# Performance work log

Hardware: AMD Instinct MI355X
Metric: run time of the kernel (lower is better)

Reference implementation:

```python
import jax, jax.numpy as jnp
import numpy as np

B, C, H, W = 4, 256, 32, 32
N_HEADS, N_GROUPS = 8, 4
HEAD_C = C // N_HEADS            # 32
GROUP_C = C // N_GROUPS          # 64
GROUP_HEADS = N_HEADS // N_GROUPS  # 2
OFFSET_RANGE_FACTOR = 4.0
SCALE = HEAD_C ** -0.5
EPS = 1e-5


def grid_sample(img, grid):
    """Bilinear grid_sample, align_corners=True, zeros padding.
    img: (N, Ch, Hi, Wi); grid: (N, Hg, Wg, 2) with (x, y) in [-1, 1]."""
    N, Ch, Hi, Wi = img.shape
    x = (grid[..., 0] + 1.0) * 0.5 * (Wi - 1)
    y = (grid[..., 1] + 1.0) * 0.5 * (Hi - 1)
    x0 = jnp.floor(x); y0 = jnp.floor(y)
    x1 = x0 + 1.0; y1 = y0 + 1.0
    wx1 = x - x0; wx0 = 1.0 - wx1
    wy1 = y - y0; wy0 = 1.0 - wy1
    img_flat = img.reshape(N, Ch, Hi * Wi)

    def corner(xi, yi, w):
        valid = (xi >= 0) & (xi <= Wi - 1) & (yi >= 0) & (yi <= Hi - 1)
        xc = jnp.clip(xi, 0, Wi - 1).astype(jnp.int32)
        yc = jnp.clip(yi, 0, Hi - 1).astype(jnp.int32)
        idx = yc * Wi + xc  # (N, Hg, Wg)
        vals = jax.vmap(lambda im, ix: im[:, ix])(img_flat, idx)  # (N, Ch, Hg, Wg)
        return vals * (w * valid)[:, None, :, :]

    return (corner(x0, y0, wx0 * wy0) + corner(x1, y0, wx1 * wy0)
            + corner(x0, y1, wx0 * wy1) + corner(x1, y1, wx1 * wy1))


def setup_inputs() -> dict:
    key = jax.random.key(0)
    ks = jax.random.split(key, 12)
    s = C ** -0.5
    return {
        "q_feat": jax.random.normal(ks[0], (B, C, H, W), jnp.float32),
        "kv_feat": jax.random.normal(ks[1], (B, C, H, W), jnp.float32),
        "Wq": jax.random.normal(ks[2], (C, C), jnp.float32) * s,
        "bq": jnp.zeros((C,), jnp.float32),
        "Wk": jax.random.normal(ks[3], (C, C), jnp.float32) * s,
        "bk": jnp.zeros((C,), jnp.float32),
        "Wv": jax.random.normal(ks[4], (C, C), jnp.float32) * s,
        "bv": jnp.zeros((C,), jnp.float32),
        "Wo": jax.random.normal(ks[5], (C, C), jnp.float32) * s,
        "bo": jnp.zeros((C,), jnp.float32),
        "off_dw_w": jax.random.normal(ks[6], (GROUP_C, 1, 3, 3), jnp.float32) / 3.0,
        "off_dw_b": jnp.zeros((GROUP_C,), jnp.float32),
        "off_ln_w": jnp.ones((GROUP_C,), jnp.float32),
        "off_ln_b": jnp.zeros((GROUP_C,), jnp.float32),
        "off_pw_w": jax.random.normal(ks[7], (2, GROUP_C), jnp.float32) * GROUP_C ** -0.5,
        "rpe_table": jax.random.normal(ks[8], (N_HEADS, 2 * H - 1, 2 * W - 1), jnp.float32) * 0.01,
    }


def reference(q_feat, kv_feat, Wq, bq, Wk, bk, Wv, bv, Wo, bo,
              off_dw_w, off_dw_b, off_ln_w, off_ln_b, off_pw_w, rpe_table):
    Bg = B * N_GROUPS
    n = H * W
    # q projection (1x1 conv)
    q = jnp.einsum('oi,bihw->bohw', Wq, q_feat) + bq[:, None, None]
    # offset network on grouped q
    q_off = q.reshape(Bg, GROUP_C, H, W)
    x = jax.lax.conv_general_dilated(q_off, off_dw_w, (1, 1), ((1, 1), (1, 1)),
                                     feature_group_count=GROUP_C,
                                     dimension_numbers=('NCHW', 'OIHW', 'NCHW'))
    x = x + off_dw_b[:, None, None]
    mu = x.mean(1, keepdims=True)
    var = x.var(1, keepdims=True)
    x = (x - mu) / jnp.sqrt(var + EPS) * off_ln_w[:, None, None] + off_ln_b[:, None, None]
    x = jax.nn.gelu(x, approximate=False)
    offset = jnp.einsum('oc,bchw->bohw', off_pw_w, x)  # (Bg, 2, H, W), (y, x)
    off_range = jnp.array([1.0 / (H - 1), 1.0 / (W - 1)], jnp.float32).reshape(1, 2, 1, 1)
    offset = jnp.tanh(offset) * off_range * OFFSET_RANGE_FACTOR
    offset = offset.transpose(0, 2, 3, 1)  # (Bg, H, W, 2)
    # reference points in [-1, 1]
    ref_y = (jnp.linspace(0.5, H - 0.5, H) / (H - 1.0)) * 2.0 - 1.0
    ref_x = (jnp.linspace(0.5, W - 0.5, W) / (W - 1.0)) * 2.0 - 1.0
    ref = jnp.stack(jnp.meshgrid(ref_y, ref_x, indexing='ij'), -1)  # (H, W, 2)
    pos = offset + ref[None]  # (Bg, H, W, 2), (y, x), no clamp (offset_range_factor >= 0)
    # deformable sampling of kv features
    kv_g = kv_feat.reshape(Bg, GROUP_C, H, W)
    x_sampled = grid_sample(kv_g, pos[..., ::-1]).reshape(B, C, n)
    k = jnp.einsum('oi,bin->bon', Wk, x_sampled) + bk[:, None]
    v = jnp.einsum('oi,bin->bon', Wv, x_sampled) + bv[:, None]
    qf = q.reshape(B, N_HEADS, HEAD_C, n)
    kf = k.reshape(B, N_HEADS, HEAD_C, n)
    vf = v.reshape(B, N_HEADS, HEAD_C, n)
    attn = jnp.einsum('bhcm,bhcn->bhmn', qf, kf) * SCALE
    # relative-position bias via bilinear sampling of rpe table
    gy = (jnp.arange(H, dtype=jnp.float32) / (H - 1.0)) * 2.0 - 1.0
    gx = (jnp.arange(W, dtype=jnp.float32) / (W - 1.0)) * 2.0 - 1.0
    q_grid = jnp.stack(jnp.meshgrid(gy, gx, indexing='ij'), -1).reshape(n, 2)
    pos_flat = pos.reshape(Bg, n, 2)
    disp = (q_grid[None, :, None, :] - pos_flat[:, None, :, :]) * 0.5  # (Bg, m, n, 2)
    rpe = jnp.broadcast_to(
        rpe_table.reshape(1, N_GROUPS, GROUP_HEADS, 2 * H - 1, 2 * W - 1),
        (B, N_GROUPS, GROUP_HEADS, 2 * H - 1, 2 * W - 1)
    ).reshape(Bg, GROUP_HEADS, 2 * H - 1, 2 * W - 1)
    bias = grid_sample(rpe, disp[..., ::-1])  # (Bg, GROUP_HEADS, m, n)
    attn = attn + bias.reshape(B, N_HEADS, n, n)
    attn = jax.nn.softmax(attn, axis=-1)
    out = jnp.einsum('bhmn,bhcn->bhcm', attn, vf).reshape(B, C, H, W)
    out = jnp.einsum('oi,bihw->bohw', Wo, out) + bo[:, None, None]
    return out
```

## Files before the change

### kernel.cpp

```cpp
#include <hip/hip_runtime.h>
#include <hip/hip_bf16.h>
#include <math.h>
#include <stdint.h>

#define BB 4
#define CC 256
#define HH 32
#define WW 32
#define NPIX 1024
#define NHEADS 8
#define NGROUPS 4
#define HEADC 32
#define GROUPC 64
#define BG 16
#define RPE_N 3969
#define SCALE_QK 0.17677669529663687f
#define LN_EPS 1e-5f

#define W_Q   0
#define W_POS 1048576
#define W_XS  1081344
#define W_KT  2129920
#define W_VV  2654208
#define W_AO  3178496
#define W_RPE 4227072
#define W_WSP 4264608

#define RPE_PACKED 4692

using frag  = __attribute__((ext_vector_type(8))) short;
using f32x4 = __attribute__((ext_vector_type(4))) float;

struct InPtrs { const void* p[16]; };

__device__ __forceinline__ float tof(float x){ return x; }
__device__ __forceinline__ float tof(__hip_bfloat16 x){ return __bfloat162float(x); }
__device__ __forceinline__ short bfs(float v) {
  __hip_bfloat16 h = __float2bfloat16(v);
  return *(short*)&h;
}
__device__ __forceinline__ bool is_f32(const void* lnw) {
  return *(const unsigned int*)lnw == 0x3F800000u;
}
__device__ __forceinline__ float ldm(const void* p, size_t i, bool f32m) {
  return f32m ? ((const float*)p)[i] : __bfloat162float(((const __hip_bfloat16*)p)[i]);
}
__device__ __forceinline__ float lof(uint32_t g){ return __uint_as_float(g << 16); }
__device__ __forceinline__ float hif(uint32_t g){ return __uint_as_float(g & 0xffff0000u); }

__global__ __launch_bounds__(512)
void prep_kernel(InPtrs ip, uint32_t* __restrict__ rpeg,
                 unsigned short* __restrict__ wsp) {
  bool f32m = is_f32(ip.p[12]);
  int blk = blockIdx.x;
  int tid = threadIdx.x;
  if (blk < 8) {
    int h = blk;
    const size_t rbase = (size_t)h * RPE_N;
    uint32_t* dst = rpeg + (size_t)h * RPE_PACKED;
    for (int i = tid; i < 68 * 69; i += 512) {
      int r = i / 69, c = i - r * 69;
      int y = r - 3, x = c - 3;
      bool yv = (y >= 0) & (y < 63);
      float va = (yv & (x >= 0) & (x < 63)) ? ldm(ip.p[15], rbase + y * 63 + x, f32m) : 0.0f;
      float vb2 = (yv & (x >= -1) & (x < 62)) ? ldm(ip.p[15], rbase + y * 63 + x + 1, f32m) : 0.0f;
      __hip_bfloat16 ha = __float2bfloat16(va), hb = __float2bfloat16(vb2);
      dst[i] = (uint32_t)*(unsigned short*)&ha | ((uint32_t)*(unsigned short*)&hb << 16);
    }
  } else {
    int wb = blk - 8;
    const void* srcs[4] = { ip.p[2], ip.p[4], ip.p[6], ip.p[8] };
    int idx0 = wb * 4096 + tid * 8;
    int m = idx0 >> 16, e0 = idx0 & 65535;
    const void* src = srcs[m];
    unsigned short* hi = wsp + (size_t)m * 131072;
    unsigned short* lo = hi + 65536;
    #pragma unroll
    for (int j = 0; j < 8; ++j) {
      float w = ldm(src, e0 + j, f32m);
      __hip_bfloat16 h = __float2bfloat16(w);
      hi[e0 + j] = *(unsigned short*)&h;
      lo[e0 + j] = (unsigned short)bfs(w - __bfloat162float(h));
    }
  }
}

template<int TM>
__device__ __forceinline__ void gemm_body(const void* xsrc, bool xf32,
    const unsigned short* __restrict__ wsp, int b, int o0, int mb,
    short* Bs, f32x4* acc) {
  const int tid = threadIdx.x;
  const int wave = tid >> 6, lane = tid & 63, quad = lane >> 4, l15 = lane & 15;
  const int og = wave & 3, mh = wave >> 2;
  const int MS = TM >> 5;
  const int NE = TM >> 4;

  size_t gbase[NE];
  int lbase[NE];
  #pragma unroll
  for (int it = 0; it < NE; ++it) {
    int i = tid + 512 * it;
    int mm = i & (TM - 1), kk = i / TM;
    gbase[it] = ((size_t)(b * CC + kk)) * NPIX + mb + mm;
    lbase[it] = mm * 72 + ((((kk >> 3) ^ (mm & 3))) << 4) + (kk & 7);
  }

  float v[NE];
  #pragma unroll
  for (int it = 0; it < NE; ++it)
    v[it] = xf32 ? ((const float*)xsrc)[gbase[it]]
                 : __bfloat162float(((const __hip_bfloat16*)xsrc)[gbase[it]]);

  for (int s = 0; s < 8; ++s) {
    short* buf = Bs + (s & 1) * (TM * 72);
    #pragma unroll
    for (int it = 0; it < NE; ++it) {
      __hip_bfloat16 h = __float2bfloat16(v[it]);
      buf[lbase[it]] = *(short*)&h;
      buf[lbase[it] + 8] = bfs(v[it] - __bfloat162float(h));
    }
    if (s < 7) {
      size_t koff = (size_t)(s + 1) * 32 * NPIX;
      #pragma unroll
      for (int it = 0; it < NE; ++it)
        v[it] = xf32 ? ((const float*)xsrc)[gbase[it] + koff]
                     : __bfloat162float(((const __hip_bfloat16*)xsrc)[gbase[it] + koff]);
    }
    const int k0 = s * 32;
    size_t wofs = (size_t)(o0 + og * 16 + l15) * CC + k0 + quad * 8;
    frag wh = *(const frag*)(wsp + wofs);
    frag wl = *(const frag*)(wsp + 65536 + wofs);
    __syncthreads();
    #pragma unroll
    for (int ms = 0; ms < MS; ++ms) {
      int ml = mh * (TM >> 1) + ms * 16 + l15;
      const short* bp = buf + ml * 72 + ((quad ^ (ml & 3)) << 4);
      frag bh = *(const frag*)bp;
      frag bl = *(const frag*)(bp + 8);
      acc[ms] = __builtin_amdgcn_mfma_f32_16x16x32_bf16(wh, bh, acc[ms], 0, 0, 0);
      acc[ms] = __builtin_amdgcn_mfma_f32_16x16x32_bf16(wh, bl, acc[ms], 0, 0, 0);
      acc[ms] = __builtin_amdgcn_mfma_f32_16x16x32_bf16(wl, bh, acc[ms], 0, 0, 0);
    }
  }
}

__global__ __launch_bounds__(512)
void qproj_kernel(InPtrs ip, const unsigned short* __restrict__ wsp,
                  float* __restrict__ q) {
  __shared__ __align__(16) short Bs[2 * 32 * 72];
  bool f32m = is_f32(ip.p[12]);
  int mb = blockIdx.x * 32, o0 = blockIdx.y * 64, b = blockIdx.z;
  int tid = threadIdx.x;
  int wave = tid >> 6, lane = tid & 63, quad = lane >> 4, l15 = lane & 15;
  f32x4 acc[1] = {{0.f,0.f,0.f,0.f}};
  gemm_body<32>(ip.p[0], f32m, wsp, b, o0, mb, Bs, acc);
  int og = wave & 3, mh = wave >> 2;
  int od = o0 + og * 16 + quad * 4;
  float bv[4];
  #pragma unroll
  for (int r = 0; r < 4; ++r) bv[r] = ldm(ip.p[3], od + r, f32m);
  int m = mb + mh * 16 + l15;
  #pragma unroll
  for (int r = 0; r < 4; ++r)
    q[(size_t)(b * CC + od + r) * NPIX + m] = acc[0][r] + bv[r];
}

__global__ __launch_bounds__(512)
void kvproj_kernel(InPtrs ip, const unsigned short* __restrict__ wspal,
                   const float* __restrict__ xs,
                   __hip_bfloat16* __restrict__ kT, __hip_bfloat16* __restrict__ vbf) {
  __shared__ __align__(16) char arena[2 * 64 * 72 * 2];
  bool f32m = is_f32(ip.p[12]);
  int mt = blockIdx.x, ot = blockIdx.y, b = blockIdx.z;
  int mb = mt * 64;
  bool isV = (ot >= 4);
  int o0 = (ot & 3) * 64;
  const unsigned short* wsp = wspal + (size_t)(isV ? 2 : 1) * 131072;
  const void* braw = isV ? ip.p[7] : ip.p[5];
  int tid = threadIdx.x;
  int wave = tid >> 6, lane = tid & 63, quad = lane >> 4, l15 = lane & 15;
  f32x4 acc[2] = {{0.f,0.f,0.f,0.f},{0.f,0.f,0.f,0.f}};
  gemm_body<64>(xs, true, wsp, b, o0, mb, (short*)arena, acc);
  int og = wave & 3, mh = wave >> 2;
  int od = o0 + og * 16 + quad * 4;
  float bv[4];
  #pragma unroll
  for (int r = 0; r < 4; ++r) bv[r] = ldm(braw, od + r, f32m);
  if (isV) {
    #pragma unroll
    for (int ms = 0; ms < 2; ++ms) {
      int m = mb + mh * 32 + ms * 16 + l15;
      #pragma unroll
      for (int r = 0; r < 4; ++r)
        vbf[(size_t)(b * CC + od + r) * NPIX + m] = __float2bfloat16(acc[ms][r] + bv[r]);
    }
  } else {
    __syncthreads();
    float* Ds = (float*)arena;
    #pragma unroll
    for (int ms = 0; ms < 2; ++ms) {
      int ml = mh * 32 + ms * 16 + l15;
      #pragma unroll
      for (int r = 0; r < 4; ++r)
        Ds[(og * 16 + quad * 4 + r) * 65 + ml] = acc[ms][r] + bv[r];
    }
    __syncthreads();
    int ot4 = ot & 3;
    {
      int q2 = tid;
      int m = q2 >> 3, cc = q2 & 7;
      __hip_bfloat16 t8[8];
      #pragma unroll
      for (int j = 0; j < 8; ++j)
        t8[j] = __float2bfloat16(Ds[(cc * 8 + j) * 65 + m]);
      int h = ot4 * 2 + (cc >> 2);
      size_t addr = ((size_t)(b * NHEADS + h) * NPIX + mb + m) * HEADC + (cc & 3) * 8;
      *(uint4*)((short*)kT + addr) = *(const uint4*)t8;
    }
  }
}

__global__ __launch_bounds__(512)
void oproj_kernel(InPtrs ip, const unsigned short* __restrict__ wsp,
                  const float* __restrict__ ao, void* __restrict__ out) {
  __shared__ __align__(16) short Bs[2 * 32 * 72];
  bool f32m = is_f32(ip.p[12]);
  int mb = blockIdx.x * 32, o0 = blockIdx.y * 64, b = blockIdx.z;
  int tid = threadIdx.x;
  int wave = tid >> 6, lane = tid & 63, quad = lane >> 4, l15 = lane & 15;
  f32x4 acc[1] = {{0.f,0.f,0.f,0.f}};
  gemm_body<32>(ao, true, wsp, b, o0, mb, Bs, acc);
  int og = wave & 3, mh = wave >> 2;
  int od = o0 + og * 16 + quad * 4;
  float bv[4];
  #pragma unroll
  for (int r = 0; r < 4; ++r) bv[r] = ldm(ip.p[9], od + r, f32m);
  int m = mb + mh * 16 + l15;
  #pragma unroll
  for (int r = 0; r < 4; ++r) {
    float val = acc[0][r] + bv[r];
    size_t idx = (size_t)(b * CC + od + r) * NPIX + m;
    if (f32m) ((float*)out)[idx] = val;
    else      ((__hip_bfloat16*)out)[idx] = __float2bfloat16(val);
  }
}

template<typename T>
__device__ __forceinline__ float tap4(const T* __restrict__ img,
                                      int x0, int y0,
                                      float wx0, float wx1, float wy0, float wy1) {
  bool xv0 = (x0 >= 0) & (x0 < WW);
  bool xv1 = (x0 >= -1) & (x0 < WW - 1);
  bool yv0 = (y0 >= 0) & (y0 < HH);
  bool yv1 = (y0 >= -1) & (y0 < HH - 1);
  float acc = 0.0f;
  if (xv0 & yv0) acc += wx0 * wy0 * tof(img[y0 * WW + x0]);
  if (xv1 & yv0) acc += wx1 * wy0 * tof(img[y0 * WW + x0 + 1]);
  if (xv0 & yv1) acc += wx0 * wy1 * tof(img[(y0 + 1) * WW + x0]);
  if (xv1 & yv1) acc += wx1 * wy1 * tof(img[(y0 + 1) * WW + x0 + 1]);
  return acc;
}

__global__ __launch_bounds__(512)
void offsample_kernel(InPtrs ip, const float* __restrict__ q,
                      float* __restrict__ pos, float* __restrict__ xs) {
  __shared__ float qs[96][65];
  __shared__ float posl[64];
  bool f32m = is_f32(ip.p[12]);
  int blk = blockIdx.x;
  int hh = blk & 31, bg = blk >> 5;
  int b = bg >> 2, g = bg & 3;
  int tid = threadIdx.x;
  const float* qg = q + (size_t)(b * CC + g * GROUPC) * NPIX;
  #pragma unroll
  for (int k = 0; k < 12; ++k) {
    int idx = tid + 512 * k;
    int ww = idx & 31, c = (idx >> 5) & 63, r3 = idx >> 11;
    int yy = hh - 1 + r3;
    float v = (yy >= 0 && yy < HH) ? qg[(size_t)c * NPIX + yy * WW + ww] : 0.0f;
    qs[r3 * 32 + ww][c] = v;
  }
  __syncthreads();
  {
    int wave = tid >> 6, c = tid & 63;
    float wdw[9];
    #pragma unroll
    for (int j = 0; j < 9; ++j) wdw[j] = ldm(ip.p[10], c * 9 + j, f32m);
    float bdw = ldm(ip.p[11], c, f32m);
    float lnw = ldm(ip.p[12], c, f32m), lnb = ldm(ip.p[13], c, f32m);
    float pwy = ldm(ip.p[14], c, f32m), pwx = ldm(ip.p[14], GROUPC + c, f32m);

    for (int p4 = 0; p4 < 4; ++p4) {
      int ww = wave * 4 + p4;
      float x = bdw;
      #pragma unroll
      for (int dy = 0; dy < 3; ++dy)
        #pragma unroll
        for (int dx = 0; dx < 3; ++dx) {
          int xx = ww + dx - 1;
          if (xx >= 0 && xx < WW) x += wdw[dy * 3 + dx] * qs[dy * 32 + xx][c];
        }
      float s = x, s2 = x * x;
      #pragma unroll
      for (int off = 32; off > 0; off >>= 1) {
        s  += __shfl_xor(s,  off);
        s2 += __shfl_xor(s2, off);
      }
      float mu  = s * (1.0f / 64.0f);
      float var = s2 * (1.0f / 64.0f) - mu * mu;
      float xn = (x - mu) * (1.0f / sqrtf(var + LN_EPS)) * lnw + lnb;
      float ge = 0.5f * xn * (1.0f + erff(xn * 0.70710678118654752f));
      float oy = pwy * ge, ox = pwx * ge;
      #pragma unroll
      for (int off = 32; off > 0; off >>= 1) {
        oy += __shfl_xor(oy, off);
        ox += __shfl_xor(ox, off);
      }
      if (c == 0) {
        float fy = tanhf(oy) * (4.0f / 31.0f);
        float fx = tanhf(ox) * (4.0f / 31.0f);
        float ry = ((0.5f + (float)hh) / 31.0f) * 2.0f - 1.0f;
        float rx = ((0.5f + (float)ww) / 31.0f) * 2.0f - 1.0f;
        float py = fy + ry, px = fx + rx;
        int m = hh * 32 + ww;
        pos[((size_t)bg * NPIX + m) * 2 + 0] = py;
        pos[((size_t)bg * NPIX + m) * 2 + 1] = px;
        posl[ww * 2 + 0] = py;
        posl[ww * 2 + 1] = px;
      }
    }
  }
  __syncthreads();
  #pragma unroll
  for (int k = 0; k < 4; ++k) {
    int s = tid + 512 * k;
    int ww = s & 31, c = (s >> 5) & 63;
    float py = posl[ww * 2 + 0], px = posl[ww * 2 + 1];
    float xi = (px + 1.0f) * 15.5f, yi = (py + 1.0f) * 15.5f;
    float x0f = floorf(xi), y0f = floorf(yi);
    float wx1 = xi - x0f, wx0 = 1.0f - wx1;
    float wy1 = yi - y0f, wy0 = 1.0f - wy1;
    int x0 = (int)x0f, y0 = (int)y0f;
    size_t img_off = (size_t)(b * CC + g * GROUPC + c) * NPIX;
    float acc;
    if (f32m) acc = tap4((const float*)ip.p[1] + img_off, x0, y0, wx0, wx1, wy0, wy1);
    else      acc = tap4((const __hip_bfloat16*)ip.p[1] + img_off, x0, y0, wx0, wx1, wy0, wy1);
    xs[img_off + hh * 32 + ww] = acc;
  }
}

__global__ __launch_bounds__(512, 3)
void attn_mfma_kernel(InPtrs ip, const uint32_t* __restrict__ rpeg,
                      const float* __restrict__ q,
                      const __hip_bfloat16* __restrict__ kT,
                      const __hip_bfloat16* __restrict__ vbf,
                      const float* __restrict__ pos, float* __restrict__ ao) {
  __shared__ __align__(16) uint32_t Du[RPE_PACKED];
  __shared__ __align__(16) __hip_bfloat16 Pw[8][16][72];
  __shared__ __align__(16) __hip_bfloat16 qA[16][40];
  __shared__ float redmax[8 * 16];
  __shared__ float redsum[8 * 16];

  int bh = blockIdx.x;
  int b = bh >> 3, h = bh & 7;
  int m0 = blockIdx.y * 16;
  int tid = threadIdx.x;
  int bg = b * 4 + (h >> 1);

  size_t slice = (size_t)(b * CC + h * HEADC) * NPIX;
  const short* kTb = (const short*)kT + (size_t)bh * NPIX * HEADC;
  const short* vb = (const short*)vbf + slice;
  const float* qb = q + slice;
  const float* posb = pos + (size_t)bg * NPIX * 2;

  {
    const uint4* src = (const uint4*)(rpeg + (size_t)h * RPE_PACKED);
    uint4* dst = (uint4*)Du;
    for (int i = tid; i < 1173; i += 512) dst[i] = src[i];
  }
  {
    int r = tid & 15, c = tid >> 4;
    qA[r][c] = __float2bfloat16(qb[(size_t)c * NPIX + m0 + r] * SCALE_QK);
  }
  __syncthreads();

  int wave = tid >> 6, lane = tid & 63;
  int quad = lane >> 4, l15 = lane & 15;
  int nbase = wave * 128;

  frag aq = *(const frag*)&qA[l15][quad * 8];
  float ybase = 31.0f + 15.5f * ((float)(m0 >> 5) * (2.0f / 31.0f) - 1.0f);
  float xbase0 = 31.0f + 15.5f * ((float)(m0 & 31) * (2.0f / 31.0f) - 1.0f);

  float pm[4], ps[4];
  f32x4 acc0 = {0.f,0.f,0.f,0.f}, acc1 = {0.f,0.f,0.f,0.f};
  #pragma unroll
  for (int reg = 0; reg < 4; ++reg) { pm[reg] = -1e30f; ps[reg] = 0.0f; }

  #pragma unroll
  for (int half = 0; half < 2; ++half) {
    int hbase = nbase + half * 64;
    float sreg[4][4];
    #pragma unroll
    for (int t8 = 0; t8 < 4; ++t8) {
      int n = hbase + t8 * 16 + l15;
      frag bk = *(const frag*)(kTb + (size_t)n * HEADC + quad * 8);
      f32x4 d = __builtin_amdgcn_mfma_f32_16x16x32_bf16(aq, bk, (f32x4){0.f,0.f,0.f,0.f}, 0, 0, 0);
      float2 pp = *(const float2*)(posb + 2 * n);
      float yi = ybase - 15.5f * pp.x;
      float y0f = floorf(yi);
      float wy1 = yi - y0f, wy0 = 1.0f - wy1;
      float xi0 = xbase0 - 15.5f * pp.y;
      float x0f = floorf(xi0);
      float wx1 = xi0 - x0f, wx0 = 1.0f - wx1;
      int row = (int)y0f + 3;
      int col = (int)x0f + 3 + quad * 4;
      const uint32_t* Dp = Du + row * 69 + col;
      uint32_t g0 = Dp[0],  g1 = Dp[2],  g2 = Dp[4];
      uint32_t h0 = Dp[69], h1 = Dp[71], h2 = Dp[73];
      float u[5];
      u[0] = wy0 * lof(g0) + wy1 * lof(h0);
      u[1] = wy0 * hif(g0) + wy1 * hif(h0);
      u[2] = wy0 * lof(g1) + wy1 * lof(h1);
      u[3] = wy0 * hif(g1) + wy1 * hif(h1);
      u[4] = wy0 * lof(g2) + wy1 * lof(h2);
      #pragma unroll
      for (int reg = 0; reg < 4; ++reg)
        sreg[t8][reg] = d[reg] + wx0 * u[reg] + wx1 * u[reg + 1];
    }
    #pragma unroll
    for (int reg = 0; reg < 4; ++reg) {
      float m = fmaxf(fmaxf(sreg[0][reg], sreg[1][reg]),
                      fmaxf(sreg[2][reg], sreg[3][reg]));
      m = fmaxf(m, __shfl_xor(m, 1));
      m = fmaxf(m, __shfl_xor(m, 2));
      m = fmaxf(m, __shfl_xor(m, 4));
      m = fmaxf(m, __shfl_xor(m, 8));
      float newm = fmaxf(pm[reg], m);
      float sc = __expf(pm[reg] - newm);
      pm[reg] = newm;
      ps[reg] *= sc;
      acc0[reg] *= sc;
      acc1[reg] *= sc;
    }
    #pragma unroll
    for (int t8 = 0; t8 < 4; ++t8) {
      #pragma unroll
      for (int reg = 0; reg < 4; ++reg) {
        float p = __expf(sreg[t8][reg] - pm[reg]);
        Pw[wave][quad * 4 + reg][t8 * 16 + l15] = __float2bfloat16(p);
        ps[reg] += p;
      }
    }
    #pragma unroll
    for (int ks = 0; ks < 2; ++ks) {
      int koff = hbase + ks * 32 + quad * 8;
      frag ap = *(const frag*)&Pw[wave][l15][ks * 32 + quad * 8];
      frag bv0 = *(const frag*)(vb + (size_t)l15 * NPIX + koff);
      frag bv1 = *(const frag*)(vb + (size_t)(16 + l15) * NPIX + koff);
      acc0 = __builtin_amdgcn_mfma_f32_16x16x32_bf16(ap, bv0, acc0, 0, 0, 0);
      acc1 = __builtin_amdgcn_mfma_f32_16x16x32_bf16(ap, bv1, acc1, 0, 0, 0);
    }
  }

  #pragma unroll
  for (int reg = 0; reg < 4; ++reg) {
    ps[reg] += __shfl_xor(ps[reg], 1);
    ps[reg] += __shfl_xor(ps[reg], 2);
    ps[reg] += __shfl_xor(ps[reg], 4);
    ps[reg] += __shfl_xor(ps[reg], 8);
  }
  if (l15 == 0) {
    #pragma unroll
    for (int reg = 0; reg < 4; ++reg) {
      redmax[wave * 16 + quad * 4 + reg] = pm[reg];
      redsum[wave * 16 + quad * 4 + reg] = ps[reg];
    }
  }
  __syncthreads();

  float* part = (float*)&Pw[0][0][0];
  {
    int e0 = (0 * 16 + l15) * 16 + quad * 4;
    int e1 = (1 * 16 + l15) * 16 + quad * 4;
    #pragma unroll
    for (int reg = 0; reg < 4; ++reg) {
      part[wave * 512 + e0 + reg] = acc0[reg];
      part[wave * 512 + e1 + reg] = acc1[reg];
    }
  }
  __syncthreads();

  {
    int c = tid >> 4, r = tid & 15;
    float M = -1e30f;
    #pragma unroll
    for (int w2 = 0; w2 < 8; ++w2) M = fmaxf(M, redmax[w2 * 16 + r]);
    float num = 0.0f, den = 0.0f;
    #pragma unroll
    for (int w2 = 0; w2 < 8; ++w2) {
      float sc = __expf(redmax[w2 * 16 + r] - M);
      num += part[w2 * 512 + tid] * sc;
      den += redsum[w2 * 16 + r] * sc;
    }
    ao[slice + (size_t)c * NPIX + m0 + r] = num / den;
  }
}

extern "C" void kernel_launch(void* const* d_in, const int* in_sizes, int n_in,
                              void* d_out, int out_size, void* d_ws, size_t ws_size,
                              hipStream_t stream) {
  float* ws  = (float*)d_ws;
  float* q   = ws + W_Q;
  float* pos = ws + W_POS;
  float* xs  = ws + W_XS;
  __hip_bfloat16* kT  = (__hip_bfloat16*)(ws + W_KT);
  __hip_bfloat16* vbf = (__hip_bfloat16*)(ws + W_VV);
  float* ao  = ws + W_AO;
  uint32_t* rpeg = (uint32_t*)(ws + W_RPE);
  unsigned short* wsp = (unsigned short*)(ws + W_WSP);

  InPtrs ip;
  for (int i = 0; i < 16; ++i) ip.p[i] = d_in[i];

  prep_kernel<<<72, 512, 0, stream>>>(ip, rpeg, wsp);
  qproj_kernel<<<dim3(32, 4, 4), 512, 0, stream>>>(ip, wsp, q);
  offsample_kernel<<<BG * 32, 512, 0, stream>>>(ip, q, pos, xs);
  kvproj_kernel<<<dim3(16, 8, 4), 512, 0, stream>>>(ip, wsp, xs, kT, vbf);
  attn_mfma_kernel<<<dim3(32, 64), 512, 0, stream>>>(ip, rpeg, q, kT, vbf, pos, ao);
  oproj_kernel<<<dim3(32, 4, 4), 512, 0, stream>>>(ip, wsp + (size_t)3 * 131072, ao, d_out);
}
```

Measured before the change: 180.0 us.

## Pre-split GEMM activations into bf16 hi/lo planes at producer kernels

Producers (prep for q_feat, offsample for sampled kv, attention for its output) now write activations as separate bf16 high and low planes instead of fp32. The GEMM body then loads two 16-bit values and stores them straight to LDS, dropping the per-tile float-to-bf16 split in every projection block. The offset-network layer norm also batches its four pixel reductions so the shuffles interleave. This adds extra prep blocks and reuses the kT workspace region for the split q_feat, which relies on kT being written only after qproj has consumed it.

```diff
diff --git a/kernel.cpp b/kernel.cpp
--- a/kernel.cpp
+++ b/kernel.cpp
@@ -27,6 +27,7 @@
 #define W_WSP 4264608
 
 #define RPE_PACKED 4692
+#define PLANE (1u << 20)
 
 using frag  = __attribute__((ext_vector_type(8))) short;
 using f32x4 = __attribute__((ext_vector_type(4))) float;
@@ -35,10 +36,6 @@
 
 __device__ __forceinline__ float tof(float x){ return x; }
 __device__ __forceinline__ float tof(__hip_bfloat16 x){ return __bfloat162float(x); }
-__device__ __forceinline__ short bfs(float v) {
-  __hip_bfloat16 h = __float2bfloat16(v);
-  return *(short*)&h;
-}
 __device__ __forceinline__ bool is_f32(const void* lnw) {
   return *(const unsigned int*)lnw == 0x3F800000u;
 }
@@ -47,10 +44,17 @@
 }
 __device__ __forceinline__ float lof(uint32_t g){ return __uint_as_float(g << 16); }
 __device__ __forceinline__ float hif(uint32_t g){ return __uint_as_float(g & 0xffff0000u); }
+__device__ __forceinline__ void split16(float v, unsigned short* ph, unsigned short* pl) {
+  __hip_bfloat16 h = __float2bfloat16(v);
+  *ph = *(unsigned short*)&h;
+  __hip_bfloat16 l = __float2bfloat16(v - __bfloat162float(h));
+  *pl = *(unsigned short*)&l;
+}
 
 __global__ __launch_bounds__(512)
 void prep_kernel(InPtrs ip, uint32_t* __restrict__ rpeg,
-                 unsigned short* __restrict__ wsp) {
+                 unsigned short* __restrict__ wsp,
+                 unsigned short* __restrict__ qf) {
   bool f32m = is_f32(ip.p[12]);
   int blk = blockIdx.x;
   int tid = threadIdx.x;
@@ -67,7 +71,7 @@
       __hip_bfloat16 ha = __float2bfloat16(va), hb = __float2bfloat16(vb2);
       dst[i] = (uint32_t)*(unsigned short*)&ha | ((uint32_t)*(unsigned short*)&hb << 16);
     }
-  } else {
+  } else if (blk < 72) {
     int wb = blk - 8;
     const void* srcs[4] = { ip.p[2], ip.p[4], ip.p[6], ip.p[8] };
     int idx0 = wb * 4096 + tid * 8;
@@ -78,15 +82,22 @@
     #pragma unroll
     for (int j = 0; j < 8; ++j) {
       float w = ldm(src, e0 + j, f32m);
-      __hip_bfloat16 h = __float2bfloat16(w);
-      hi[e0 + j] = *(unsigned short*)&h;
-      lo[e0 + j] = (unsigned short)bfs(w - __bfloat162float(h));
+      split16(w, &hi[e0 + j], &lo[e0 + j]);
+    }
+  } else {
+    int wb2 = blk - 72;
+    int e0 = wb2 * 4096 + tid * 8;
+    #pragma unroll
+    for (int j = 0; j < 8; ++j) {
+      float w = ldm(ip.p[0], e0 + j, f32m);
+      split16(w, &qf[e0 + j], &qf[PLANE + e0 + j]);
     }
   }
 }
 
 template<int TM>
-__device__ __forceinline__ void gemm_body(const void* xsrc, bool xf32,
+__device__ __forceinline__ void gemm_body(const unsigned short* __restrict__ xh,
+    const unsigned short* __restrict__ xl,
     const unsigned short* __restrict__ wsp, int b, int o0, int mb,
     short* Bs, f32x4* acc) {
   const int tid = threadIdx.x;
@@ -105,26 +116,27 @@
     lbase[it] = mm * 72 + ((((kk >> 3) ^ (mm & 3))) << 4) + (kk & 7);
   }
 
-  float v[NE];
-  #pragma unroll
-  for (int it = 0; it < NE; ++it)
-    v[it] = xf32 ? ((const float*)xsrc)[gbase[it]]
-                 : __bfloat162float(((const __hip_bfloat16*)xsrc)[gbase[it]]);
+  unsigned short vh[NE], vl[NE];
+  #pragma unroll
+  for (int it = 0; it < NE; ++it) {
+    vh[it] = xh[gbase[it]];
+    vl[it] = xl[gbase[it]];
+  }
 
   for (int s = 0; s < 8; ++s) {
     short* buf = Bs + (s & 1) * (TM * 72);
     #pragma unroll
     for (int it = 0; it < NE; ++it) {
-      __hip_bfloat16 h = __float2bfloat16(v[it]);
-      buf[lbase[it]] = *(short*)&h;
-      buf[lbase[it] + 8] = bfs(v[it] - __bfloat162float(h));
+      buf[lbase[it]] = (short)vh[it];
+      buf[lbase[it] + 8] = (short)vl[it];
     }
     if (s < 7) {
       size_t koff = (size_t)(s + 1) * 32 * NPIX;
       #pragma unroll
-      for (int it = 0; it < NE; ++it)
-        v[it] = xf32 ? ((const float*)xsrc)[gbase[it] + koff]
-                     : __bfloat162float(((const __hip_bfloat16*)xsrc)[gbase[it] + koff]);
+      for (int it = 0; it < NE; ++it) {
+        vh[it] = xh[gbase[it] + koff];
+        vl[it] = xl[gbase[it] + koff];
+      }
     }
     const int k0 = s * 32;
     size_t wofs = (size_t)(o0 + og * 16 + l15) * CC + k0 + quad * 8;
@@ -145,7 +157,8 @@
 }
 
 __global__ __launch_bounds__(512)
-void qproj_kernel(InPtrs ip, const unsigned short* __restrict__ wsp,
+void qproj_kernel(InPtrs ip, const unsigned short* __restrict__ qf,
+                  const unsigned short* __restrict__ wsp,
                   float* __restrict__ q) {
   __shared__ __align__(16) short Bs[2 * 32 * 72];
   bool f32m = is_f32(ip.p[12]);
@@ -153,7 +166,7 @@
   int tid = threadIdx.x;
   int wave = tid >> 6, lane = tid & 63, quad = lane >> 4, l15 = lane & 15;
   f32x4 acc[1] = {{0.f,0.f,0.f,0.f}};
-  gemm_body<32>(ip.p[0], f32m, wsp, b, o0, mb, Bs, acc);
+  gemm_body<32>(qf, qf + PLANE, wsp, b, o0, mb, Bs, acc);
   int og = wave & 3, mh = wave >> 2;
   int od = o0 + og * 16 + quad * 4;
   float bv[4];
@@ -166,8 +179,8 @@
 }
 
 __global__ __launch_bounds__(512)
-void kvproj_kernel(InPtrs ip, const unsigned short* __restrict__ wspal,
-                   const float* __restrict__ xs,
+void kvproj_kernel(InPtrs ip, const unsigned short* __restrict__ xsp,
+                   const unsigned short* __restrict__ wspal,
                    __hip_bfloat16* __restrict__ kT, __hip_bfloat16* __restrict__ vbf) {
   __shared__ __align__(16) char arena[2 * 64 * 72 * 2];
   bool f32m = is_f32(ip.p[12]);
@@ -180,7 +193,7 @@
   int tid = threadIdx.x;
   int wave = tid >> 6, lane = tid & 63, quad = lane >> 4, l15 = lane & 15;
   f32x4 acc[2] = {{0.f,0.f,0.f,0.f},{0.f,0.f,0.f,0.f}};
-  gemm_body<64>(xs, true, wsp, b, o0, mb, (short*)arena, acc);
+  gemm_body<64>(xsp, xsp + PLANE, wsp, b, o0, mb, (short*)arena, acc);
   int og = wave & 3, mh = wave >> 2;
   int od = o0 + og * 16 + quad * 4;
   float bv[4];
@@ -221,15 +234,15 @@
 }
 
 __global__ __launch_bounds__(512)
-void oproj_kernel(InPtrs ip, const unsigned short* __restrict__ wsp,
-                  const float* __restrict__ ao, void* __restrict__ out) {
+void oproj_kernel(InPtrs ip, const unsigned short* __restrict__ aop,
+                  const unsigned short* __restrict__ wsp, void* __restrict__ out) {
   __shared__ __align__(16) short Bs[2 * 32 * 72];
   bool f32m = is_f32(ip.p[12]);
   int mb = blockIdx.x * 32, o0 = blockIdx.y * 64, b = blockIdx.z;
   int tid = threadIdx.x;
   int wave = tid >> 6, lane = tid & 63, quad = lane >> 4, l15 = lane & 15;
   f32x4 acc[1] = {{0.f,0.f,0.f,0.f}};
-  gemm_body<32>(ao, true, wsp, b, o0, mb, Bs, acc);
+  gemm_body<32>(aop, aop + PLANE, wsp, b, o0, mb, Bs, acc);
   int og = wave & 3, mh = wave >> 2;
   int od = o0 + og * 16 + quad * 4;
   float bv[4];
@@ -263,7 +276,7 @@
 
 __global__ __launch_bounds__(512)
 void offsample_kernel(InPtrs ip, const float* __restrict__ q,
-                      float* __restrict__ pos, float* __restrict__ xs) {
+                      float* __restrict__ pos, unsigned short* __restrict__ xsp) {
   __shared__ float qs[96][65];
   __shared__ float posl[64];
   bool f32m = is_f32(ip.p[12]);
@@ -290,8 +303,10 @@
     float lnw = ldm(ip.p[12], c, f32m), lnb = ldm(ip.p[13], c, f32m);
     float pwy = ldm(ip.p[14], c, f32m), pwx = ldm(ip.p[14], GROUPC + c, f32m);
 
-    for (int p4 = 0; p4 < 4; ++p4) {
-      int ww = wave * 4 + p4;
+    float xv[4];
+    #pragma unroll
+    for (int p = 0; p < 4; ++p) {
+      int ww = wave * 4 + p;
       float x = bdw;
       #pragma unroll
       for (int dy = 0; dy < 3; ++dy)
@@ -300,25 +315,40 @@
           int xx = ww + dx - 1;
           if (xx >= 0 && xx < WW) x += wdw[dy * 3 + dx] * qs[dy * 32 + xx][c];
         }
-      float s = x, s2 = x * x;
-      #pragma unroll
-      for (int off = 32; off > 0; off >>= 1) {
-        s  += __shfl_xor(s,  off);
-        s2 += __shfl_xor(s2, off);
+      xv[p] = x;
+    }
+    float sA[4], s2A[4];
+    #pragma unroll
+    for (int p = 0; p < 4; ++p) { sA[p] = xv[p]; s2A[p] = xv[p] * xv[p]; }
+    #pragma unroll
+    for (int off = 32; off > 0; off >>= 1)
+      #pragma unroll
+      for (int p = 0; p < 4; ++p) {
+        sA[p]  += __shfl_xor(sA[p],  off);
+        s2A[p] += __shfl_xor(s2A[p], off);
       }
-      float mu  = s * (1.0f / 64.0f);
-      float var = s2 * (1.0f / 64.0f) - mu * mu;
-      float xn = (x - mu) * (1.0f / sqrtf(var + LN_EPS)) * lnw + lnb;
+    float oyA[4], oxA[4];
+    #pragma unroll
+    for (int p = 0; p < 4; ++p) {
+      float mu  = sA[p] * (1.0f / 64.0f);
+      float var = s2A[p] * (1.0f / 64.0f) - mu * mu;
+      float xn = (xv[p] - mu) * (1.0f / sqrtf(var + LN_EPS)) * lnw + lnb;
       float ge = 0.5f * xn * (1.0f + erff(xn * 0.70710678118654752f));
-      float oy = pwy * ge, ox = pwx * ge;
-      #pragma unroll
-      for (int off = 32; off > 0; off >>= 1) {
-        oy += __shfl_xor(oy, off);
-        ox += __shfl_xor(ox, off);
+      oyA[p] = pwy * ge; oxA[p] = pwx * ge;
+    }
+    #pragma unroll
+    for (int off = 32; off > 0; off >>= 1)
+      #pragma unroll
+      for (int p = 0; p < 4; ++p) {
+        oyA[p] += __shfl_xor(oyA[p], off);
+        oxA[p] += __shfl_xor(oxA[p], off);
       }
-      if (c == 0) {
-        float fy = tanhf(oy) * (4.0f / 31.0f);
-        float fx = tanhf(ox) * (4.0f / 31.0f);
+    if (c == 0) {
+      #pragma unroll
+      for (int p = 0; p < 4; ++p) {
+        int ww = wave * 4 + p;
+        float fy = tanhf(oyA[p]) * (4.0f / 31.0f);
+        float fx = tanhf(oxA[p]) * (4.0f / 31.0f);
         float ry = ((0.5f + (float)hh) / 31.0f) * 2.0f - 1.0f;
         float rx = ((0.5f + (float)ww) / 31.0f) * 2.0f - 1.0f;
         float py = fy + ry, px = fx + rx;
@@ -345,7 +375,8 @@
     float acc;
     if (f32m) acc = tap4((const float*)ip.p[1] + img_off, x0, y0, wx0, wx1, wy0, wy1);
     else      acc = tap4((const __hip_bfloat16*)ip.p[1] + img_off, x0, y0, wx0, wx1, wy0, wy1);
-    xs[img_off + hh * 32 + ww] = acc;
+    size_t oidx = img_off + hh * 32 + ww;
+    split16(acc, &xsp[oidx], &xsp[PLANE + oidx]);
   }
 }
 
@@ -354,7 +385,8 @@
                       const float* __restrict__ q,
                       const __hip_bfloat16* __restrict__ kT,
                       const __hip_bfloat16* __restrict__ vbf,
-                      const float* __restrict__ pos, float* __restrict__ ao) {
+                      const float* __restrict__ pos,
+                      unsigned short* __restrict__ aop) {
   __shared__ __align__(16) uint32_t Du[RPE_PACKED];
   __shared__ __align__(16) __hip_bfloat16 Pw[8][16][72];
   __shared__ __align__(16) __hip_bfloat16 qA[16][40];
@@ -503,7 +535,8 @@
       num += part[w2 * 512 + tid] * sc;
       den += redsum[w2 * 16 + r] * sc;
     }
-    ao[slice + (size_t)c * NPIX + m0 + r] = num / den;
+    size_t oidx = slice + (size_t)c * NPIX + m0 + r;
+    split16(num / den, &aop[oidx], &aop[PLANE + oidx]);
   }
 }
 
@@ -513,20 +546,21 @@
   float* ws  = (float*)d_ws;
   float* q   = ws + W_Q;
   float* pos = ws + W_POS;
-  float* xs  = ws + W_XS;
+  unsigned short* xsp = (unsigned short*)(ws + W_XS);
   __hip_bfloat16* kT  = (__hip_bfloat16*)(ws + W_KT);
   __hip_bfloat16* vbf = (__hip_bfloat16*)(ws + W_VV);
-  float* ao  = ws + W_AO;
+  unsigned short* aop = (unsigned short*)(ws + W_AO);
   uint32_t* rpeg = (uint32_t*)(ws + W_RPE);
   unsigned short* wsp = (unsigned short*)(ws + W_WSP);
+  unsigned short* qf = (unsigned short*)(ws + W_KT);
 
   InPtrs ip;
   for (int i = 0; i < 16; ++i) ip.p[i] = d_in[i];
 
-  prep_kernel<<<72, 512, 0, stream>>>(ip, rpeg, wsp);
-  qproj_kernel<<<dim3(32, 4, 4), 512, 0, stream>>>(ip, wsp, q);
-  offsample_kernel<<<BG * 32, 512, 0, stream>>>(ip, q, pos, xs);
-  kvproj_kernel<<<dim3(16, 8, 4), 512, 0, stream>>>(ip, wsp, xs, kT, vbf);
-  attn_mfma_kernel<<<dim3(32, 64), 512, 0, stream>>>(ip, rpeg, q, kT, vbf, pos, ao);
-  oproj_kernel<<<dim3(32, 4, 4), 512, 0, stream>>>(ip, wsp + (size_t)3 * 131072, ao, d_out);
-}
+  prep_kernel<<<328, 512, 0, stream>>>(ip, rpeg, wsp, qf);
+  qproj_kernel<<<dim3(32, 4, 4), 512, 0, stream>>>(ip, qf, wsp, q);
+  offsample_kernel<<<BG * 32, 512, 0, stream>>>(ip, q, pos, xsp);
+  kvproj_kernel<<<dim3(16, 8, 4), 512, 0, stream>>>(ip, xsp, wsp, kT, vbf);
+  attn_mfma_kernel<<<dim3(32, 64), 512, 0, stream>>>(ip, rpeg, q, kT, vbf, pos, aop);
+  oproj_kernel<<<dim3(32, 4, 4), 512, 0, stream>>>(ip, aop, wsp + (size_t)3 * 131072, d_out);
+}
```

Result: no change. 181.9 us (+1.0%).
